# Performance work log

Measured on AMD Instinct MI355X. Metric: run time of the kernel, lower is better.

The kernel has to match this reference:

```python
import jax, jax.numpy as jnp
import numpy as np

N = 100000   # nodes
E = 800000   # directed edges (dst sorted)
D = 64       # input_dim
H = 64       # hidden_dim (must equal input_dim per fusion_layer shape)
L = 16       # latent_dim


def _lin(k, fan_in, fan_out):
    # torch nn.Linear-like init scale
    bound = 1.0 / np.sqrt(fan_in)
    kw, kb = jax.random.split(k)
    W = jax.random.uniform(kw, (fan_in, fan_out), jnp.float32, -bound, bound)
    b = jax.random.uniform(kb, (fan_out,), jnp.float32, -bound, bound)
    return W, b


def setup_inputs() -> dict:
    key = jax.random.key(0)
    ks = jax.random.split(key, 12)
    x = jax.random.normal(ks[0], (N, D), jnp.float32)
    edge_src = jax.random.randint(ks[1], (E,), 0, N, jnp.int32)
    edge_dst = jnp.sort(jax.random.randint(ks[2], (E,), 0, N, jnp.int32))
    eps = jax.random.normal(ks[3], (N, L), jnp.float32)
    W_agg, b_agg = _lin(ks[4], D, H)          # neighbor_aggregator
    W_fus, b_fus = _lin(ks[5], 2 * H, H)      # fusion_layer
    W1, b1 = _lin(ks[6], H, H)                # fc1 (input_dim==hidden_dim)
    W21, b21 = _lin(ks[7], H, L)              # fc21 -> mu
    W22, b22 = _lin(ks[8], H, L)              # fc22 -> logvar
    W3, b3 = _lin(ks[9], L, H)                # fc3
    W4, b4 = _lin(ks[10], H, D)               # fc4
    return {"x": x, "edge_src": edge_src, "edge_dst": edge_dst, "eps": eps,
            "W_agg": W_agg, "b_agg": b_agg, "W_fus": W_fus, "b_fus": b_fus,
            "W1": W1, "b1": b1, "W21": W21, "b21": b21,
            "W22": W22, "b22": b22, "W3": W3, "b3": b3, "W4": W4, "b4": b4}


def reference(x, edge_src, edge_dst, eps, W_agg, b_agg, W_fus, b_fus,
              W1, b1, W21, b21, W22, b22, W3, b3, W4, b4):
    n = x.shape[0]
    # aggregate_neighbors: segment-mean over variable-length neighbor lists;
    # nodes with no neighbors get zeros (sum==0, count clamped to 1).
    nsum = jax.ops.segment_sum(x[edge_src], edge_dst, num_segments=n)
    cnt = jax.ops.segment_sum(jnp.ones((edge_dst.shape[0],), x.dtype), edge_dst, num_segments=n)
    neighbor_avg = nsum / jnp.maximum(cnt, 1.0)[:, None]          # [N, D]
    neighbor_encoded = jax.nn.relu(neighbor_avg @ W_agg + b_agg)   # [N, H]
    combined = jnp.concatenate([x, neighbor_encoded], axis=1)      # [N, 2H]
    xf = jax.nn.relu(combined @ W_fus + b_fus)                     # [N, H]
    # VAE encode
    h1 = jax.nn.relu(xf @ W1 + b1)
    mu = h1 @ W21 + b21
    logvar = h1 @ W22 + b22
    # reparameterize (fixed eps for determinism)
    z = mu + eps * jnp.exp(0.5 * logvar)
    # decode
    h3 = jax.nn.relu(z @ W3 + b3)
    recon = jax.nn.sigmoid(h3 @ W4 + b4)
    return (recon, mu, logvar)
```

## Files before the change

kernel.cpp:

```cpp
#include <hip/hip_runtime.h>
#include <math.h>

#define N_NODES 100000
#define E_EDGES 800000
#define NT 16
#define NTILES (N_NODES / NT)
#define OFF_MU 6400000L
#define OFF_LV 8000000L

typedef __attribute__((ext_vector_type(8))) short short8;
typedef __attribute__((ext_vector_type(4))) float f32x4;
typedef __attribute__((ext_vector_type(4))) float float4v;

#define SW_AGG 0
#define SW_FUS 4096
#define SW_W1  12288
#define SW_W2  16384
#define SW_W3  18432
#define SW_W4  20480
#define SW_TOT 24576

#define PW_OFF (1 << 20)
#define XB_OFF (2 << 20)

#define PB_RS 3125
#define PB_W  7
#define PB_X  3125

__device__ __forceinline__ unsigned short f2bf(float f) {
    unsigned u = __float_as_uint(f);
    unsigned r = u + 0x7FFFu + ((u >> 16) & 1u);
    return (unsigned short)(r >> 16);
}
__device__ __forceinline__ float bf2f(unsigned short h) {
    return __uint_as_float(((unsigned)h) << 16);
}

__device__ __forceinline__ int pidx(int row, int col) {
    const int c = ((col >> 3) ^ (row & 7));
    return row * 64 + c * 8 + (col & 7);
}

__device__ void stage_w(const float* __restrict__ W, int Ksrc, int NC,
                        int NKT, int NJT_local, int jt_off,
                        int rb, short* sw, int tid) {
    const int tot = NJT_local * NKT * 64;
    for (int s = tid; s < tot; s += 256) {
        int f = s >> 6, l = s & 63;
        int jtl = f / NKT, kt = f - jtl * NKT;
        int col = jtl * 16 + (l & 15);
        int k0 = kt * 32 + ((l >> 4) << 3);
        short8 hi;
        #pragma unroll
        for (int i = 0; i < 8; ++i) {
            float v = (k0 + i < Ksrc) ? W[(k0 + i) * NC + col] : 0.0f;
            hi[i] = (short)f2bf(v);
        }
        int fg = (jt_off + jtl) * NKT + kt;
        *(short8*)&sw[rb + fg * 512 + l * 8] = hi;
    }
}

__global__ __launch_bounds__(256) void prep(
    const int* __restrict__ edge_dst, int* __restrict__ row_start,
    const float* __restrict__ W_agg, const float* __restrict__ W_fus,
    const float* __restrict__ W1,  const float* __restrict__ W21,
    const float* __restrict__ W22, const float* __restrict__ W3,
    const float* __restrict__ W4, short* __restrict__ gw,
    const float* __restrict__ x, short* __restrict__ xbf)
{
    const int b = blockIdx.x;
    const int tid = threadIdx.x;
    if (b < PB_RS) {
        const int e = b * 256 + tid;
        if (e >= E_EDGES) return;
        int d = edge_dst[e];
        int dprev = (e == 0) ? -1 : edge_dst[e - 1];
        for (int n = dprev + 1; n <= d; ++n) row_start[n] = e;
        if (e == E_EDGES - 1) {
            for (int n = d + 1; n <= N_NODES; ++n) row_start[n] = E_EDGES;
        }
    } else if (b < PB_RS + PB_W) {
        switch (b - PB_RS) {
            case 0: stage_w(W_agg, 64, 64, 2, 4, 0, SW_AGG, gw, tid); break;
            case 1: stage_w(W_fus, 128, 64, 4, 4, 0, SW_FUS, gw, tid); break;
            case 2: stage_w(W1,   64, 64, 2, 4, 0, SW_W1,  gw, tid); break;
            case 3: stage_w(W21,  64, 16, 2, 1, 0, SW_W2,  gw, tid); break;
            case 4: stage_w(W22,  64, 16, 2, 1, 1, SW_W2,  gw, tid); break;
            case 5: stage_w(W3,   16, 64, 1, 4, 0, SW_W3,  gw, tid); break;
            case 6: stage_w(W4,   64, 64, 2, 4, 0, SW_W4,  gw, tid); break;
        }
    } else {
        const int i = (b - PB_RS - PB_W) * 256 + tid;
        if (i >= N_NODES * 8) return;
        const float4v a = ((const float4v*)x)[i * 2];
        const float4v c = ((const float4v*)x)[i * 2 + 1];
        short8 s;
        s[0] = (short)f2bf(a.x); s[1] = (short)f2bf(a.y);
        s[2] = (short)f2bf(a.z); s[3] = (short)f2bf(a.w);
        s[4] = (short)f2bf(c.x); s[5] = (short)f2bf(c.y);
        s[6] = (short)f2bf(c.z); s[7] = (short)f2bf(c.w);
        ((short8*)xbf)[i] = s;
    }
}

__device__ __forceinline__ void frags_from_xbf(const short* __restrict__ xbf,
                                               long base, int lane, short8* h) {
    const int row = lane & 15, ko = (lane >> 4) * 8;
    const short* r = xbf + (base + row) * 64;
    h[0] = *(const short8*)&r[ko];
    h[1] = *(const short8*)&r[32 + ko];
}

template<int NKT>
__device__ __forceinline__ void frags_from_planes(const short* phi, int lane,
                                                  short8* hi) {
    const int row = lane & 15;
    #pragma unroll
    for (int kt = 0; kt < NKT; ++kt) {
        const int c = kt * 4 + (lane >> 4);
        const int idx = row * 64 + ((c ^ (row & 7)) << 3);
        hi[kt] = *(const short8*)&phi[idx];
    }
}

template<int NKT>
__device__ __forceinline__ f32x4 gemm_one(const short8* ah,
                                          const short* __restrict__ sw, int rb,
                                          int jt, float bias, int lane) {
    f32x4 acc = { bias, bias, bias, bias };
    #pragma unroll
    for (int kt = 0; kt < NKT; ++kt) {
        const short8 bhi = *(const short8*)&sw[rb + (jt * NKT + kt) * 512 + lane * 8];
        acc = __builtin_amdgcn_mfma_f32_16x16x32_bf16(ah[kt], bhi, acc, 0, 0, 0);
    }
    return acc;
}

__device__ __forceinline__ void write_slab_plane(short* phi, f32x4 c, int jt,
                                                 int lane, bool relu) {
    const int g = lane >> 4, cj = lane & 15;
    const int col = jt * 16 + cj;
    #pragma unroll
    for (int r = 0; r < 4; ++r) {
        float f = relu ? fmaxf(c[r], 0.0f) : c[r];
        phi[pidx(g * 4 + r, col)] = (short)f2bf(f);
    }
}

__device__ __forceinline__ float tree16(const float* v) {
    float a0 = (v[0] + v[1]) + (v[2] + v[3]);
    float a1 = (v[4] + v[5]) + (v[6] + v[7]);
    float a2 = (v[8] + v[9]) + (v[10] + v[11]);
    float a3 = (v[12] + v[13]) + (v[14] + v[15]);
    return (a0 + a1) + (a2 + a3);
}
__device__ __forceinline__ float tree8(const float* v) {
    return ((v[0] + v[1]) + (v[2] + v[3])) + ((v[4] + v[5]) + (v[6] + v[7]));
}

__global__ __launch_bounds__(256, 8) void vae_top(
    const short* __restrict__ xbf,
    const int* __restrict__ edge_src,
    const float* __restrict__ eps,
    const float* __restrict__ b_agg, const float* __restrict__ b_fus,
    const float* __restrict__ b1,  const float* __restrict__ b21,
    const float* __restrict__ b22, const float* __restrict__ b3,
    const float* __restrict__ b4,
    const short* __restrict__ gw,
    const int* __restrict__ row_start,
    float* __restrict__ out)
{
    __shared__ __align__(16) short sA[1024];
    __shared__ __align__(16) short sB[1024];
    __shared__ __align__(16) short sZ[4 * 16 * 24];

    const int tid  = threadIdx.x;
    const int lane = tid & 63;
    const int wid  = tid >> 6;
    const long base = (long)blockIdx.x * NT;
    const int cj = lane & 15, g = lane >> 4;

    const float bja = b_agg[wid * 16 + cj];
    const float bjf = b_fus[wid * 16 + cj];
    const float bj1 = b1[wid * 16 + cj];
    const float bj3 = b3[wid * 16 + cj];
    const float bj4 = b4[wid * 16 + cj];
    const float b21l = b21[cj];
    const float b22l = b22[cj];

    const unsigned short* xbu = (const unsigned short*)xbf;
    short* sZw = sZ + wid * (16 * 24);

    {
        const int rsv = row_start[(int)base + (lane < 17 ? lane : 16)];
        const int W0 = __builtin_amdgcn_readlane(rsv, wid * 4);
        int p0 = W0 + lane;      p0 = p0 < E_EDGES ? p0 : E_EDGES - 1;
        int p1 = W0 + 64 + lane; p1 = p1 < E_EDGES ? p1 : E_EDGES - 1;
        const int iv0 = edge_src[p0];
        const int iv1 = edge_src[p1];

        #pragma unroll
        for (int q = 0; q < 4; ++q) {
            const int node = wid * 4 + q;
            const int e0 = __builtin_amdgcn_readlane(rsv, node);
            const int e1 = __builtin_amdgcn_readlane(rsv, node + 1);
            const int deg = e1 - e0;
            const int te0 = e0 - W0;
            float sum;
            if (deg <= 8 && te0 + 7 < 128) {
                float v[8];
                #pragma unroll
                for (int i = 0; i < 8; ++i) {
                    const int te = te0 + i;
                    const int vsel = (te & 64) ? iv1 : iv0;
                    int ix = __builtin_amdgcn_readlane(vsel, te & 63);
                    const bool live = i < deg;
                    ix = live ? ix : 0;
                    float tv = bf2f(xbu[(long)ix * 64 + lane]);
                    v[i] = live ? tv : 0.0f;
                }
                sum = tree8(v);
            } else if (te0 + 15 < 128) {
                float v[16];
                #pragma unroll
                for (int i = 0; i < 16; ++i) {
                    const int te = te0 + i;
                    const int vsel = (te & 64) ? iv1 : iv0;
                    int ix = __builtin_amdgcn_readlane(vsel, te & 63);
                    const bool live = i < deg;
                    ix = live ? ix : 0;
                    float tv = bf2f(xbu[(long)ix * 64 + lane]);
                    v[i] = live ? tv : 0.0f;
                }
                sum = tree16(v);
                for (int e = e0 + 16; e < e1; ++e)
                    sum += bf2f(xbu[(long)edge_src[e] * 64 + lane]);
            } else {
                float v[16];
                #pragma unroll
                for (int i = 0; i < 16; ++i) {
                    const int ee = e0 + i;
                    const bool live = ee < e1;
                    const int ec = ee < E_EDGES ? ee : E_EDGES - 1;
                    int ix = edge_src[ec];
                    ix = live ? ix : 0;
                    float tv = bf2f(xbu[(long)ix * 64 + lane]);
                    v[i] = live ? tv : 0.0f;
                }
                sum = tree16(v);
                for (int e = e0 + 16; e < e1; ++e)
                    sum += bf2f(xbu[(long)edge_src[e] * 64 + lane]);
            }
            const float avg = sum / fmaxf((float)deg, 1.0f);
            sA[pidx(node, lane)] = (short)f2bf(avg);
        }
    }
    __syncthreads();

    short8 ah[4];
    f32x4 c;

    frags_from_planes<2>(sA, lane, ah);
    c = gemm_one<2>(ah, gw, SW_AGG, wid, bja, lane);
    write_slab_plane(sB, c, wid, lane, true);
    __syncthreads();

    frags_from_xbf(xbf, base, lane, ah);
    frags_from_planes<2>(sB, lane, ah + 2);
    c = gemm_one<4>(ah, gw, SW_FUS, wid, bjf, lane);
    write_slab_plane(sA, c, wid, lane, true);
    __syncthreads();

    frags_from_planes<2>(sA, lane, ah);
    c = gemm_one<2>(ah, gw, SW_W1, wid, bj1, lane);
    write_slab_plane(sB, c, wid, lane, true);
    __syncthreads();

    {
        frags_from_planes<2>(sB, lane, ah);
        const f32x4 cmu = gemm_one<2>(ah, gw, SW_W2, 0, b21l, lane);
        const f32x4 clv = gemm_one<2>(ah, gw, SW_W2, 1, b22l, lane);
        #pragma unroll
        for (int r = 0; r < 4; ++r) {
            const long node = base + g * 4 + r;
            if (wid == 0) {
                out[OFF_MU + node * 16 + cj] = cmu[r];
                out[OFF_LV + node * 16 + cj] = clv[r];
            }
            const float z = cmu[r] + eps[node * 16 + cj] * __expf(0.5f * clv[r]);
            sZw[(g * 4 + r) * 24 + cj] = (short)f2bf(z);
        }
    }

    {
        short8 zh = {0,0,0,0,0,0,0,0};
        if (lane < 32) {
            const int row = lane & 15;
            const int ch = lane >> 4;
            zh = *(const short8*)&sZw[row * 24 + ch * 8];
        }
        c = gemm_one<1>(&zh, gw, SW_W3, wid, bj3, lane);
    }
    write_slab_plane(sA, c, wid, lane, true);
    __syncthreads();

    frags_from_planes<2>(sA, lane, ah);
    c = gemm_one<2>(ah, gw, SW_W4, wid, bj4, lane);
    #pragma unroll
    for (int r = 0; r < 4; ++r) {
        const float s = 1.0f / (1.0f + __expf(-c[r]));
        out[(base + g * 4 + r) * 64 + wid * 16 + cj] = s;
    }
}

extern "C" void kernel_launch(void* const* d_in, const int* in_sizes, int n_in,
                              void* d_out, int out_size, void* d_ws, size_t ws_size,
                              hipStream_t stream) {
    const float* x        = (const float*)d_in[0];
    const int*   edge_src = (const int*)  d_in[1];
    const int*   edge_dst = (const int*)  d_in[2];
    const float* eps      = (const float*)d_in[3];
    const float* W_agg    = (const float*)d_in[4];
    const float* b_agg    = (const float*)d_in[5];
    const float* W_fus    = (const float*)d_in[6];
    const float* b_fus    = (const float*)d_in[7];
    const float* W1       = (const float*)d_in[8];
    const float* b1       = (const float*)d_in[9];
    const float* W21      = (const float*)d_in[10];
    const float* b21      = (const float*)d_in[11];
    const float* W22      = (const float*)d_in[12];
    const float* b22      = (const float*)d_in[13];
    const float* W3       = (const float*)d_in[14];
    const float* b3       = (const float*)d_in[15];
    const float* W4       = (const float*)d_in[16];
    const float* b4       = (const float*)d_in[17];
    float* out = (float*)d_out;

    int*   row_start = (int*)d_ws;
    short* gw        = (short*)((char*)d_ws + PW_OFF);
    short* xbf       = (short*)((char*)d_ws + XB_OFF);

    prep<<<PB_RS + PB_W + PB_X, 256, 0, stream>>>(edge_dst, row_start,
                                                  W_agg, W_fus, W1, W21, W22, W3, W4,
                                                  gw, x, xbf);
    vae_top<<<NTILES, 256, 0, stream>>>(xbf, edge_src, eps,
                                        b_agg, b_fus, b1, b21, b22, b3, b4,
                                        gw, row_start, out);
}
```

Before: 57.63 us.

## Use persistent grid-stride tiles and drop per-edge liveness selects in gather

The main kernel now launches a fixed grid of 2048 blocks that loop over the 6250 node tiles, instead of one block per tile. Bias loads are amortized across tiles and block launch overhead drops. The gather no longer zero-masks dead edge slots. Those slots load node 0, and the sum is corrected afterwards by subtracting the count of dead slots times node 0's value. This trades some loads for fewer selects but adds rounding differences, and the persistent loop adds a trailing barrier per tile and may balance the tail worse.

```diff
diff --git a/kernel.cpp b/kernel.cpp
--- a/kernel.cpp
+++ b/kernel.cpp
@@ -5,6 +5,7 @@
 #define E_EDGES 800000
 #define NT 16
 #define NTILES (N_NODES / NT)
+#define GRID 2048
 #define OFF_MU 6400000L
 #define OFF_LV 8000000L
 
@@ -178,7 +179,6 @@
     const int tid  = threadIdx.x;
     const int lane = tid & 63;
     const int wid  = tid >> 6;
-    const long base = (long)blockIdx.x * NT;
     const int cj = lane & 15, g = lane >> 4;
 
     const float bja = b_agg[wid * 16 + cj];
@@ -190,127 +190,129 @@
     const float b22l = b22[cj];
 
     const unsigned short* xbu = (const unsigned short*)xbf;
+    const float x0lane = bf2f(xbu[lane]);
     short* sZw = sZ + wid * (16 * 24);
 
-    {
-        const int rsv = row_start[(int)base + (lane < 17 ? lane : 16)];
-        const int W0 = __builtin_amdgcn_readlane(rsv, wid * 4);
-        int p0 = W0 + lane;      p0 = p0 < E_EDGES ? p0 : E_EDGES - 1;
-        int p1 = W0 + 64 + lane; p1 = p1 < E_EDGES ? p1 : E_EDGES - 1;
-        const int iv0 = edge_src[p0];
-        const int iv1 = edge_src[p1];
-
-        #pragma unroll
-        for (int q = 0; q < 4; ++q) {
-            const int node = wid * 4 + q;
-            const int e0 = __builtin_amdgcn_readlane(rsv, node);
-            const int e1 = __builtin_amdgcn_readlane(rsv, node + 1);
-            const int deg = e1 - e0;
-            const int te0 = e0 - W0;
-            float sum;
-            if (deg <= 8 && te0 + 7 < 128) {
-                float v[8];
-                #pragma unroll
-                for (int i = 0; i < 8; ++i) {
-                    const int te = te0 + i;
-                    const int vsel = (te & 64) ? iv1 : iv0;
-                    int ix = __builtin_amdgcn_readlane(vsel, te & 63);
-                    const bool live = i < deg;
-                    ix = live ? ix : 0;
-                    float tv = bf2f(xbu[(long)ix * 64 + lane]);
-                    v[i] = live ? tv : 0.0f;
+    for (int t = blockIdx.x; t < NTILES; t += GRID) {
+        const long base = (long)t * NT;
+
+        {
+            const int rsv = row_start[(int)base + (lane < 17 ? lane : 16)];
+            const int W0 = __builtin_amdgcn_readlane(rsv, wid * 4);
+            int p0 = W0 + lane;      p0 = p0 < E_EDGES ? p0 : E_EDGES - 1;
+            int p1 = W0 + 64 + lane; p1 = p1 < E_EDGES ? p1 : E_EDGES - 1;
+            const int iv0 = edge_src[p0];
+            const int iv1 = edge_src[p1];
+
+            #pragma unroll
+            for (int q = 0; q < 4; ++q) {
+                const int node = wid * 4 + q;
+                const int e0 = __builtin_amdgcn_readlane(rsv, node);
+                const int e1 = __builtin_amdgcn_readlane(rsv, node + 1);
+                const int deg = e1 - e0;
+                const int te0 = e0 - W0;
+                float sum;
+                if (deg <= 8 && te0 + 7 < 128) {
+                    float v[8];
+                    #pragma unroll
+                    for (int i = 0; i < 8; ++i) {
+                        const int te = te0 + i;
+                        const int vsel = (te & 64) ? iv1 : iv0;
+                        int ix = __builtin_amdgcn_readlane(vsel, te & 63);
+                        ix = (i < deg) ? ix : 0;
+                        v[i] = bf2f(xbu[(long)ix * 64 + lane]);
+                    }
+                    sum = tree8(v) - (float)(8 - deg) * x0lane;
+                } else if (te0 + 15 < 128) {
+                    float v[16];
+                    #pragma unroll
+                    for (int i = 0; i < 16; ++i) {
+                        const int te = te0 + i;
+                        const int vsel = (te & 64) ? iv1 : iv0;
+                        int ix = __builtin_amdgcn_readlane(vsel, te & 63);
+                        ix = (i < deg) ? ix : 0;
+                        v[i] = bf2f(xbu[(long)ix * 64 + lane]);
+                    }
+                    int dead = 16 - deg; dead = dead > 0 ? dead : 0;
+                    sum = tree16(v) - (float)dead * x0lane;
+                    for (int e = e0 + 16; e < e1; ++e)
+                        sum += bf2f(xbu[(long)edge_src[e] * 64 + lane]);
+                } else {
+                    float v[16];
+                    #pragma unroll
+                    for (int i = 0; i < 16; ++i) {
+                        const int ee = e0 + i;
+                        const int ec = ee < E_EDGES ? ee : E_EDGES - 1;
+                        int ix = edge_src[ec];
+                        ix = (i < deg) ? ix : 0;
+                        v[i] = bf2f(xbu[(long)ix * 64 + lane]);
+                    }
+                    int dead = 16 - deg; dead = dead > 0 ? dead : 0;
+                    sum = tree16(v) - (float)dead * x0lane;
+                    for (int e = e0 + 16; e < e1; ++e)
+                        sum += bf2f(xbu[(long)edge_src[e] * 64 + lane]);
                 }
-                sum = tree8(v);
-            } else if (te0 + 15 < 128) {
-                float v[16];
-                #pragma unroll
-                for (int i = 0; i < 16; ++i) {
-                    const int te = te0 + i;
-                    const int vsel = (te & 64) ? iv1 : iv0;
-                    int ix = __builtin_amdgcn_readlane(vsel, te & 63);
-                    const bool live = i < deg;
-                    ix = live ? ix : 0;
-                    float tv = bf2f(xbu[(long)ix * 64 + lane]);
-                    v[i] = live ? tv : 0.0f;
+                const float avg = sum / fmaxf((float)deg, 1.0f);
+                sA[pidx(node, lane)] = (short)f2bf(avg);
+            }
+        }
+        __syncthreads();
+
+        short8 ah[4];
+        f32x4 c;
+
+        frags_from_planes<2>(sA, lane, ah);
+        c = gemm_one<2>(ah, gw, SW_AGG, wid, bja, lane);
+        write_slab_plane(sB, c, wid, lane, true);
+        __syncthreads();
+
+        frags_from_xbf(xbf, base, lane, ah);
+        frags_from_planes<2>(sB, lane, ah + 2);
+        c = gemm_one<4>(ah, gw, SW_FUS, wid, bjf, lane);
+        write_slab_plane(sA, c, wid, lane, true);
+        __syncthreads();
+
+        frags_from_planes<2>(sA, lane, ah);
+        c = gemm_one<2>(ah, gw, SW_W1, wid, bj1, lane);
+        write_slab_plane(sB, c, wid, lane, true);
+        __syncthreads();
+
+        {
+            frags_from_planes<2>(sB, lane, ah);
+            const f32x4 cmu = gemm_one<2>(ah, gw, SW_W2, 0, b21l, lane);
+            const f32x4 clv = gemm_one<2>(ah, gw, SW_W2, 1, b22l, lane);
+            #pragma unroll
+            for (int r = 0; r < 4; ++r) {
+                const long node = base + g * 4 + r;
+                if (wid == 0) {
+                    out[OFF_MU + node * 16 + cj] = cmu[r];
+                    out[OFF_LV + node * 16 + cj] = clv[r];
                 }
-                sum = tree16(v);
-                for (int e = e0 + 16; e < e1; ++e)
-                    sum += bf2f(xbu[(long)edge_src[e] * 64 + lane]);
-            } else {
-                float v[16];
-                #pragma unroll
-                for (int i = 0; i < 16; ++i) {
-                    const int ee = e0 + i;
-                    const bool live = ee < e1;
-                    const int ec = ee < E_EDGES ? ee : E_EDGES - 1;
-                    int ix = edge_src[ec];
-                    ix = live ? ix : 0;
-                    float tv = bf2f(xbu[(long)ix * 64 + lane]);
-                    v[i] = live ? tv : 0.0f;
-                }
-                sum = tree16(v);
-                for (int e = e0 + 16; e < e1; ++e)
-                    sum += bf2f(xbu[(long)edge_src[e] * 64 + lane]);
+                const float z = cmu[r] + eps[node * 16 + cj] * __expf(0.5f * clv[r]);
+                sZw[(g * 4 + r) * 24 + cj] = (short)f2bf(z);
             }
-            const float avg = sum / fmaxf((float)deg, 1.0f);
-            sA[pidx(node, lane)] = (short)f2bf(avg);
-        }
-    }
-    __syncthreads();
-
-    short8 ah[4];
-    f32x4 c;
-
-    frags_from_planes<2>(sA, lane, ah);
-    c = gemm_one<2>(ah, gw, SW_AGG, wid, bja, lane);
-    write_slab_plane(sB, c, wid, lane, true);
-    __syncthreads();
-
-    frags_from_xbf(xbf, base, lane, ah);
-    frags_from_planes<2>(sB, lane, ah + 2);
-    c = gemm_one<4>(ah, gw, SW_FUS, wid, bjf, lane);
-    write_slab_plane(sA, c, wid, lane, true);
-    __syncthreads();
-
-    frags_from_planes<2>(sA, lane, ah);
-    c = gemm_one<2>(ah, gw, SW_W1, wid, bj1, lane);
-    write_slab_plane(sB, c, wid, lane, true);
-    __syncthreads();
-
-    {
-        frags_from_planes<2>(sB, lane, ah);
-        const f32x4 cmu = gemm_one<2>(ah, gw, SW_W2, 0, b21l, lane);
-        const f32x4 clv = gemm_one<2>(ah, gw, SW_W2, 1, b22l, lane);
+        }
+
+        {
+            short8 zh = {0,0,0,0,0,0,0,0};
+            if (lane < 32) {
+                const int row = lane & 15;
+                const int ch = lane >> 4;
+                zh = *(const short8*)&sZw[row * 24 + ch * 8];
+            }
+            c = gemm_one<1>(&zh, gw, SW_W3, wid, bj3, lane);
+        }
+        write_slab_plane(sA, c, wid, lane, true);
+        __syncthreads();
+
+        frags_from_planes<2>(sA, lane, ah);
+        c = gemm_one<2>(ah, gw, SW_W4, wid, bj4, lane);
         #pragma unroll
         for (int r = 0; r < 4; ++r) {
-            const long node = base + g * 4 + r;
-            if (wid == 0) {
-                out[OFF_MU + node * 16 + cj] = cmu[r];
-                out[OFF_LV + node * 16 + cj] = clv[r];
-            }
-            const float z = cmu[r] + eps[node * 16 + cj] * __expf(0.5f * clv[r]);
-            sZw[(g * 4 + r) * 24 + cj] = (short)f2bf(z);
-        }
-    }
-
-    {
-        short8 zh = {0,0,0,0,0,0,0,0};
-        if (lane < 32) {
-            const int row = lane & 15;
-            const int ch = lane >> 4;
-            zh = *(const short8*)&sZw[row * 24 + ch * 8];
-        }
-        c = gemm_one<1>(&zh, gw, SW_W3, wid, bj3, lane);
-    }
-    write_slab_plane(sA, c, wid, lane, true);
-    __syncthreads();
-
-    frags_from_planes<2>(sA, lane, ah);
-    c = gemm_one<2>(ah, gw, SW_W4, wid, bj4, lane);
-    #pragma unroll
-    for (int r = 0; r < 4; ++r) {
-        const float s = 1.0f / (1.0f + __expf(-c[r]));
-        out[(base + g * 4 + r) * 64 + wid * 16 + cj] = s;
+            const float s = 1.0f / (1.0f + __expf(-c[r]));
+            out[(base + g * 4 + r) * 64 + wid * 16 + cj] = s;
+        }
+        __syncthreads();
     }
 }
 
@@ -344,7 +346,7 @@
     prep<<<PB_RS + PB_W + PB_X, 256, 0, stream>>>(edge_dst, row_start,
                                                   W_agg, W_fus, W1, W21, W22, W3, W4,
                                                   gw, x, xbf);
-    vae_top<<<NTILES, 256, 0, stream>>>(xbf, edge_src, eps,
-                                        b_agg, b_fus, b1, b21, b22, b3, b4,
-                                        gw, row_start, out);
-}
+    vae_top<<<GRID, 256, 0, stream>>>(xbf, edge_src, eps,
+                                      b_agg, b_fus, b1, b21, b22, b3, b4,
+                                      gw, row_start, out);
+}
```

Measured after the change: 163.8 us. 184% more time.
